# Performance work log

Measured on AMD Instinct MI355X. Metric: run time of the kernel, lower is better.

Reference implementation:

```python
import jax, jax.numpy as jnp
import numpy as np

N_NODES = 50000
N_EDGES = 800000
IN_C, HID_C, OUT_C = 256, 512, 256
DROP_P = 0.5


def _glorot(key, fan_in, fan_out):
    lim = float(np.sqrt(6.0 / (fan_in + fan_out)))
    return jax.random.uniform(key, (fan_in, fan_out), jnp.float32, -lim, lim)


def setup_inputs() -> dict:
    key = jax.random.key(0)
    k_x, k_e, k_w1, k_w2 = jax.random.split(key, 4)
    tensor = jax.random.normal(k_x, (N_NODES, IN_C), dtype=jnp.float32)
    edge_index = jax.random.randint(k_e, (2, N_EDGES), 0, N_NODES, dtype=jnp.int64)
    W1 = _glorot(k_w1, IN_C, HID_C)
    b1 = jnp.zeros((HID_C,), jnp.float32)
    W2 = _glorot(k_w2, HID_C, OUT_C)
    b2 = jnp.zeros((OUT_C,), jnp.float32)
    return {"tensor": tensor, "edge_index": edge_index,
            "W1": W1, "b1": b1, "W2": W2, "b2": b2}


def _gcn_conv(x, W, b, row, col, n_nodes):
    # PyG GCNConv: x' = D^-1/2 (A + I) D^-1/2 (x W) + b
    x = x @ W                                            # [N, F_out]
    # degree over targets including self-loops
    deg = jax.ops.segment_sum(jnp.ones_like(col, dtype=x.dtype), col,
                              num_segments=n_nodes) + 1.0
    dinv = jnp.where(deg > 0, jax.lax.rsqrt(deg), 0.0)   # [N]
    norm = dinv[row] * dinv[col]                         # [E]
    msg = x[row] * norm[:, None]                         # [E, F_out] gather
    out = jax.ops.segment_sum(msg, col, num_segments=n_nodes)  # scatter-add
    out = out + x * (dinv * dinv)[:, None]               # self-loop term
    return out + b


def _dropout(x, key, p=DROP_P):
    keep = jax.random.bernoulli(key, 1.0 - p, x.shape)
    return jnp.where(keep, x / (1.0 - p), 0.0)


def reference(tensor, edge_index, W1, b1, W2, b2):
    row, col = edge_index[0], edge_index[1]
    k1, k2 = jax.random.split(jax.random.key(42))
    x = _gcn_conv(tensor, W1, b1, row, col, N_NODES)
    x = _dropout(jax.nn.relu(x), k1)
    x = _gcn_conv(x, W2, b2, row, col, N_NODES)
    x = _dropout(jax.nn.relu(x), k2)
    return x
```

## Files before the change

kernel.cpp:

```cpp
#include <hip/hip_runtime.h>
#include <stdint.h>


#define N_NODES 50000
#define N_EDGES 800000
#define M_PAD   50048
#define IN_C 256
#define HID_C 512
#define OUT_C 256

typedef __attribute__((ext_vector_type(8))) short bf16x8;
typedef __attribute__((ext_vector_type(4))) float f32x4;

struct U2 { unsigned a, b; };

__host__ __device__ constexpr unsigned rotl32(unsigned x, int d) {
  return (x << d) | (x >> (32 - d));
}

#define TF_ROUND(r) { x0 += x1; x1 = rotl32(x1, (r)); x1 ^= x0; }

__host__ __device__ constexpr U2 threefry2x32(unsigned k0, unsigned k1,
                                              unsigned x0, unsigned x1) {
  unsigned ks2 = k0 ^ k1 ^ 0x1BD11BDAu;
  x0 += k0; x1 += k1;
  TF_ROUND(13) TF_ROUND(15) TF_ROUND(26) TF_ROUND(6)  x0 += k1;  x1 += ks2 + 1u;
  TF_ROUND(17) TF_ROUND(29) TF_ROUND(16) TF_ROUND(24) x0 += ks2; x1 += k0 + 2u;
  TF_ROUND(13) TF_ROUND(15) TF_ROUND(26) TF_ROUND(6)  x0 += k0;  x1 += k1 + 3u;
  TF_ROUND(17) TF_ROUND(29) TF_ROUND(16) TF_ROUND(24) x0 += k1;  x1 += ks2 + 4u;
  TF_ROUND(13) TF_ROUND(15) TF_ROUND(26) TF_ROUND(6)  x0 += ks2; x1 += k0 + 5u;
  return U2{x0, x1};
}

__device__ __forceinline__ float drop_apply(float v, unsigned idx, unsigned k0, unsigned k1) {
  v = fmaxf(v, 0.f);
  U2 r = threefry2x32(k0, k1, 0u, idx);
  unsigned bits = r.a ^ r.b;
  return (bits >> 31) ? 0.f : v * 2.0f;
}

__device__ __forceinline__ ushort f2b(float f) {
  unsigned u = __builtin_bit_cast(unsigned, f);
  unsigned r = (u + 0x7fffu + ((u >> 16) & 1u)) >> 16;
  return (ushort)r;
}
__device__ __forceinline__ float b2f(ushort h) {
  unsigned u = (unsigned)h << 16;
  return __builtin_bit_cast(float, u);
}

__device__ __forceinline__ void gload16(const void* g, void* l) {
  __builtin_amdgcn_global_load_lds(
      (const __attribute__((address_space(1))) void*)g,
      (__attribute__((address_space(3))) void*)l, 16, 0, 0);
}

__global__ void deg_kernel(const int* __restrict__ col, int* __restrict__ cnt, int E) {
  int e = blockIdx.x * 256 + threadIdx.x;
  if (e < E) atomicAdd(&cnt[col[e]], 1);
}

__global__ void dinv_kernel(const int* __restrict__ cnt, float* __restrict__ dinv, int N) {
  int n = blockIdx.x * 256 + threadIdx.x;
  if (n < N) dinv[n] = rsqrtf((float)cnt[n] + 1.0f);
}

__global__ __launch_bounds__(1024) void scan_local(const int* __restrict__ cnt,
                                                   int* __restrict__ indptr,
                                                   int* __restrict__ chunkSums, int n) {
  __shared__ int s[1024];
  int gid = blockIdx.x * 1024 + threadIdx.x;
  int v = (gid < n) ? cnt[gid] : 0;
  s[threadIdx.x] = v;
  __syncthreads();
#pragma unroll
  for (int off = 1; off < 1024; off <<= 1) {
    int t = (threadIdx.x >= off) ? s[threadIdx.x - off] : 0;
    __syncthreads();
    s[threadIdx.x] += t;
    __syncthreads();
  }
  if (gid < n) indptr[gid] = s[threadIdx.x] - v;
  if (threadIdx.x == 1023) chunkSums[blockIdx.x] = s[1023];
}

__global__ void scan_chunks(int* __restrict__ chunkSums, int nChunks) {
  if (threadIdx.x == 0 && blockIdx.x == 0) {
    int acc = 0;
    for (int i = 0; i < nChunks; ++i) { int t = chunkSums[i]; chunkSums[i] = acc; acc += t; }
  }
}

__global__ void add_offsets(int* __restrict__ indptr, const int* __restrict__ chunkSums,
                            int n, int total) {
  int gid = blockIdx.x * 256 + threadIdx.x;
  if (gid < n) indptr[gid] += chunkSums[gid >> 10];
  if (gid == 0) indptr[n] = total;
}

__global__ void build_csr(const int* __restrict__ row, const int* __restrict__ col,
                          const int* __restrict__ indptr, int* __restrict__ cursor,
                          int* __restrict__ srcSorted, int E) {
  int e = blockIdx.x * 256 + threadIdx.x;
  if (e < E) {
    int c = col[e];
    int p = indptr[c] + atomicAdd(&cursor[c], 1);
    srcSorted[p] = row[e];
  }
}

__global__ void cvt_f32_bf16(const float* __restrict__ in, ushort* __restrict__ out, int n4) {
  int i = blockIdx.x * 256 + threadIdx.x;
  if (i < n4) {
    float4 v = *(const float4*)(in + (size_t)i * 4);
    ushort4 o = make_ushort4(f2b(v.x), f2b(v.y), f2b(v.z), f2b(v.w));
    *(ushort4*)(out + (size_t)i * 4) = o;
  }
}

template <int LOGK>
__global__ void wT_kernel(const float* __restrict__ W, ushort* __restrict__ WT, int N, int total) {
  int i = blockIdx.x * 256 + threadIdx.x;
  if (i < total) {
    int k = i & ((1 << LOGK) - 1);
    int n = i >> LOGK;
    WT[i] = f2b(W[(size_t)k * N + n]);
  }
}

template <bool EPI>
__global__ __launch_bounds__(256) void gather_agg16(const ushort* __restrict__ X,
                                                    const int* __restrict__ indptr,
                                                    const int* __restrict__ srcS,
                                                    const float* __restrict__ dinv,
                                                    const float* __restrict__ bias,
                                                    void* __restrict__ outp,
                                                    unsigned char* __restrict__ maskOut,
                                                    unsigned kk0, unsigned kk1, int N) {
  int wid = (blockIdx.x * 256 + threadIdx.x) >> 6;
  int lane = threadIdx.x & 63;
  if (wid >= N) return;
  int beg = __builtin_amdgcn_readfirstlane(indptr[wid]);
  int end = __builtin_amdgcn_readfirstlane(indptr[wid + 1]);
  float dc = dinv[wid];
  const int f0 = lane * 4;
  ushort4 sv = *(const ushort4*)(X + (size_t)wid * 256 + f0);
  float a0 = b2f(sv.x) * dc, a1 = b2f(sv.y) * dc,
        a2 = b2f(sv.z) * dc, a3 = b2f(sv.w) * dc;
  int e = beg;
  for (; e + 2 <= end; e += 2) {
    int r0 = srcS[e], r1 = srcS[e + 1];
    float w0 = dinv[r0], w1 = dinv[r1];
    ushort4 v0 = *(const ushort4*)(X + (size_t)r0 * 256 + f0);
    ushort4 v1 = *(const ushort4*)(X + (size_t)r1 * 256 + f0);
    a0 += b2f(v0.x) * w0; a1 += b2f(v0.y) * w0; a2 += b2f(v0.z) * w0; a3 += b2f(v0.w) * w0;
    a0 += b2f(v1.x) * w1; a1 += b2f(v1.y) * w1; a2 += b2f(v1.z) * w1; a3 += b2f(v1.w) * w1;
  }
  if (e < end) {
    int r0 = srcS[e];
    float w0 = dinv[r0];
    ushort4 v0 = *(const ushort4*)(X + (size_t)r0 * 256 + f0);
    a0 += b2f(v0.x) * w0; a1 += b2f(v0.y) * w0; a2 += b2f(v0.z) * w0; a3 += b2f(v0.w) * w0;
  }
  a0 *= dc; a1 *= dc; a2 *= dc; a3 *= dc;
  if (EPI) {
    unsigned base = (unsigned)wid * 256u + (unsigned)f0;
    a0 = drop_apply(a0 + bias[f0 + 0], base + 0, kk0, kk1);
    a1 = drop_apply(a1 + bias[f0 + 1], base + 1, kk0, kk1);
    a2 = drop_apply(a2 + bias[f0 + 2], base + 2, kk0, kk1);
    a3 = drop_apply(a3 + bias[f0 + 3], base + 3, kk0, kk1);
    *(float4*)((float*)outp + (size_t)wid * 256 + f0) = make_float4(a0, a1, a2, a3);
  } else {
    ushort4 o = make_ushort4(f2b(a0), f2b(a1), f2b(a2), f2b(a3));
    *(ushort4*)((ushort*)outp + (size_t)wid * 256 + f0) = o;
    unsigned gl = (unsigned)wid * 64u + (unsigned)lane;
    unsigned eb = gl * 8u;
    unsigned byte = 0;
#pragma unroll
    for (int j = 0; j < 8; ++j) {
      U2 r = threefry2x32(kk0, kk1, 0u, eb + (unsigned)j);
      byte |= (((r.a ^ r.b) >> 31) & 1u) << j;
    }
    maskOut[gl] = (unsigned char)byte;
  }
}

template <bool EPI>
__global__ __launch_bounds__(256) void gemm_bf16(const ushort* __restrict__ A,
                                                 const ushort* __restrict__ BT,
                                                 ushort* __restrict__ C,
                                                 int M, int K, int N,
                                                 const float* __restrict__ bias,
                                                 const unsigned char* __restrict__ mask) {
  __shared__ __align__(16) ushort lds[4 * 128 * 64];
  const int tid = threadIdx.x;
  const int lane = tid & 63;
  const int wv = tid >> 6;
  const int wr = wv >> 1, wc = wv & 1;
  const int bm = blockIdx.x * 128;
  const int bn = blockIdx.y * 128;

  f32x4 acc[4][4] = {};
  const int xorv = (lane & 7) << 4;

  auto stage = [&](int buf, int k0) {
#pragma unroll
    for (int l = 0; l < 4; ++l) {
      int cid = l * 256 + tid;
      int row = cid >> 3;
      int kcol = ((cid & 7) ^ (row & 7)) * 8;
      gload16(A + (size_t)(bm + row) * K + k0 + kcol, (void*)(lds + buf * 8192 + cid * 8));
      gload16(BT + (size_t)(bn + row) * K + k0 + kcol, (void*)(lds + (2 + buf) * 8192 + cid * 8));
    }
  };

  const int nt = K >> 6;
  stage(0, 0);
  __syncthreads();
  int cur = 0;
  for (int t = 0; t < nt; ++t) {
    if (t + 1 < nt) stage(cur ^ 1, (t + 1) << 6);
    const char* Ab = (const char*)(lds + cur * 8192);
    const char* Bb = (const char*)(lds + (2 + cur) * 8192);
#pragma unroll
    for (int ks = 0; ks < 2; ++ks) {
      bf16x8 af[4], bf[4];
      const int kb = (ks * 64 + (lane >> 4) * 16) ^ xorv;
#pragma unroll
      for (int i = 0; i < 4; ++i) {
        int arow = wr * 64 + i * 16 + (lane & 15);
        af[i] = *(const bf16x8*)(Ab + arow * 128 + kb);
        int brow = wc * 64 + i * 16 + (lane & 15);
        bf[i] = *(const bf16x8*)(Bb + brow * 128 + kb);
      }
#pragma unroll
      for (int m = 0; m < 4; ++m)
#pragma unroll
        for (int n = 0; n < 4; ++n)
          acc[m][n] = __builtin_amdgcn_mfma_f32_16x16x32_bf16(af[m], bf[n], acc[m][n], 0, 0, 0);
    }
    __syncthreads();
    cur ^= 1;
  }

  ushort* Csm = (ushort*)lds;
  const int rowoff = wr * 64 + ((lane >> 4) << 2);
  const int coloff = wc * 64 + (lane & 15);
  float bias_v[4];
  if (EPI) {
#pragma unroll
    for (int n = 0; n < 4; ++n) bias_v[n] = bias[bn + coloff + n * 16];
  }
#pragma unroll
  for (int m = 0; m < 4; ++m) {
#pragma unroll
    for (int r = 0; r < 4; ++r) {
      int lrow = rowoff + m * 16 + r;
      unsigned long long mk = 0;
      if (EPI) {
        unsigned base = (unsigned)(bm + lrow) * (unsigned)N + (unsigned)(bn + wc * 64);
        mk = *(const unsigned long long*)(mask + (base >> 3));
      }
#pragma unroll
      for (int n = 0; n < 4; ++n) {
        float v = acc[m][n][r];
        if (EPI) {
          v = fmaxf(v + bias_v[n], 0.f);
          v = ((mk >> ((lane & 15) + n * 16)) & 1ull) ? 0.f : v * 2.0f;
        }
        Csm[lrow * 132 + coloff + n * 16] = f2b(v);
      }
    }
  }
  __syncthreads();
  {
    int row = tid >> 1, ch = (tid & 1) * 64;
    const ushort* src = Csm + row * 132 + ch;
    ushort* dst = C + (size_t)(bm + row) * N + bn + ch;
#pragma unroll
    for (int j = 0; j < 8; ++j)
      *(bf16x8*)(dst + j * 8) = *(const bf16x8*)(src + j * 8);
  }
}

extern "C" void kernel_launch(void* const* d_in, const int* in_sizes, int n_in,
                              void* d_out, int out_size, void* d_ws, size_t ws_size,
                              hipStream_t stream) {
  const float* x  = (const float*)d_in[0];
  const int*   ei = (const int*)d_in[1];
  const float* W1 = (const float*)d_in[2];
  const float* b1 = (const float*)d_in[3];
  const float* W2 = (const float*)d_in[4];
  const float* b2 = (const float*)d_in[5];
  float* out = (float*)d_out;
  (void)in_sizes; (void)n_in; (void)out_size; (void)ws_size;

  const int* row = ei;
  const int* col = ei + N_EDGES;

  char* ws = (char*)d_ws;
  float*  dinv      = (float*) (ws);
  int*    cnt       = (int*)   (ws + (1u << 18));
  int*    indptr    = (int*)   (ws + (2u << 18));
  int*    cursor    = (int*)   (ws + (3u << 18));
  int*    chunkSums = (int*)   (ws + (1u << 20));
  int*    srcSorted = (int*)   (ws + (1u << 20) + (1u << 16));
  ushort* W1T       = (ushort*)(ws + 5u  * (1u << 20));
  ushort* W2T       = (ushort*)(ws + 5u  * (1u << 20) + (1u << 19));
  unsigned char* mask1 = (unsigned char*)(ws + 6u * (1u << 20));
  ushort* x16       = (ushort*)(ws + 10u * (1u << 20));
  ushort* aggB      = (ushort*)(ws + 36u * (1u << 20));
  ushort* h         = (ushort*)(ws + 64u * (1u << 20));
  ushort* hw2       = (ushort*)(ws + 116u* (1u << 20));

  constexpr U2 K1 = threefry2x32(0u, 42u, 0u, 0u);
  constexpr U2 K2 = threefry2x32(0u, 42u, 0u, 1u);

  hipMemsetAsync(cnt, 0, N_NODES * sizeof(int), stream);
  hipMemsetAsync(cursor, 0, N_NODES * sizeof(int), stream);
  deg_kernel<<<(N_EDGES + 255) / 256, 256, 0, stream>>>(col, cnt, N_EDGES);
  dinv_kernel<<<(N_NODES + 255) / 256, 256, 0, stream>>>(cnt, dinv, N_NODES);
  const int nChunks = (N_NODES + 1023) / 1024;
  scan_local<<<nChunks, 1024, 0, stream>>>(cnt, indptr, chunkSums, N_NODES);
  scan_chunks<<<1, 64, 0, stream>>>(chunkSums, nChunks);
  add_offsets<<<(N_NODES + 255) / 256, 256, 0, stream>>>(indptr, chunkSums, N_NODES, N_EDGES);
  build_csr<<<(N_EDGES + 255) / 256, 256, 0, stream>>>(row, col, indptr, cursor, srcSorted, N_EDGES);

  cvt_f32_bf16<<<(N_NODES * IN_C / 4 + 255) / 256, 256, 0, stream>>>(x, x16, N_NODES * IN_C / 4);
  wT_kernel<8><<<(IN_C * HID_C + 255) / 256, 256, 0, stream>>>(W1, W1T, HID_C, IN_C * HID_C);
  wT_kernel<9><<<(HID_C * OUT_C + 255) / 256, 256, 0, stream>>>(W2, W2T, OUT_C, HID_C * OUT_C);
  hipMemsetAsync(aggB + (size_t)N_NODES * IN_C, 0, (size_t)(M_PAD - N_NODES) * IN_C * 2, stream);

  gather_agg16<false><<<(N_NODES + 3) / 4, 256, 0, stream>>>(
      x16, indptr, srcSorted, dinv, nullptr, aggB, mask1, K1.a, K1.b, N_NODES);
  gemm_bf16<true><<<dim3(M_PAD / 128, HID_C / 128), 256, 0, stream>>>(
      aggB, W1T, h, M_PAD, IN_C, HID_C, b1, mask1);

  gemm_bf16<false><<<dim3(M_PAD / 128, OUT_C / 128), 256, 0, stream>>>(
      h, W2T, hw2, M_PAD, HID_C, OUT_C, nullptr, nullptr);
  gather_agg16<true><<<(N_NODES + 3) / 4, 256, 0, stream>>>(
      hw2, indptr, srcSorted, dinv, b2, out, nullptr, K2.a, K2.b, N_NODES);
}
```

Before: 347.4 us.

## Store gather inputs in 32-feature column chunks for cache-local SpMM

Node features that get gathered (the bf16 input and the second GEMM's output) are stored in eight column-chunked planes of 32 features per node. The gather kernel now assigns each block one chunk, so all blocks working on the same chunk touch a smaller working set that fits in L2. Within a wave, four edge slots run in parallel and are combined with shuffle reductions. The cost is 8x more blocks, each redoing the indptr, srcS and dinv reads. Each block also does narrower 4-byte loads, and the mask generation moves to a subset of blocks.

```diff
diff --git a/kernel.cpp b/kernel.cpp
--- a/kernel.cpp
+++ b/kernel.cpp
@@ -8,6 +8,7 @@
 #define IN_C 256
 #define HID_C 512
 #define OUT_C 256
+#define CH_STRIDE ((size_t)M_PAD * 32)
 
 typedef __attribute__((ext_vector_type(8))) short bf16x8;
 typedef __attribute__((ext_vector_type(4))) float f32x4;
@@ -48,6 +49,12 @@
   unsigned u = (unsigned)h << 16;
   return __builtin_bit_cast(float, u);
 }
+__device__ __forceinline__ float b2f_hi(unsigned u) {
+  return __builtin_bit_cast(float, u & 0xffff0000u);
+}
+__device__ __forceinline__ float b2f_lo(unsigned u) {
+  return __builtin_bit_cast(float, u << 16);
+}
 
 __device__ __forceinline__ void gload16(const void* g, void* l) {
   __builtin_amdgcn_global_load_lds(
@@ -109,12 +116,16 @@
   }
 }
 
-__global__ void cvt_f32_bf16(const float* __restrict__ in, ushort* __restrict__ out, int n4) {
+__global__ void cvt_chunked(const float* __restrict__ in, ushort* __restrict__ Xc, int n4) {
   int i = blockIdx.x * 256 + threadIdx.x;
   if (i < n4) {
+    int n = i >> 6;
+    int fq = (i & 63) * 4;
+    int c = fq >> 5;
+    int fi = fq & 31;
     float4 v = *(const float4*)(in + (size_t)i * 4);
     ushort4 o = make_ushort4(f2b(v.x), f2b(v.y), f2b(v.z), f2b(v.w));
-    *(ushort4*)(out + (size_t)i * 4) = o;
+    *(ushort4*)(Xc + (size_t)c * CH_STRIDE + (size_t)n * 32 + fi) = o;
   }
 }
 
@@ -129,7 +140,7 @@
 }
 
 template <bool EPI>
-__global__ __launch_bounds__(256) void gather_agg16(const ushort* __restrict__ X,
+__global__ __launch_bounds__(256) void gather_chunk(const ushort* __restrict__ Xc,
                                                     const int* __restrict__ indptr,
                                                     const int* __restrict__ srcS,
                                                     const float* __restrict__ dinv,
@@ -137,55 +148,66 @@
                                                     void* __restrict__ outp,
                                                     unsigned char* __restrict__ maskOut,
                                                     unsigned kk0, unsigned kk1, int N) {
-  int wid = (blockIdx.x * 256 + threadIdx.x) >> 6;
-  int lane = threadIdx.x & 63;
-  if (wid >= N) return;
-  int beg = __builtin_amdgcn_readfirstlane(indptr[wid]);
-  int end = __builtin_amdgcn_readfirstlane(indptr[wid + 1]);
-  float dc = dinv[wid];
-  const int f0 = lane * 4;
-  ushort4 sv = *(const ushort4*)(X + (size_t)wid * 256 + f0);
-  float a0 = b2f(sv.x) * dc, a1 = b2f(sv.y) * dc,
-        a2 = b2f(sv.z) * dc, a3 = b2f(sv.w) * dc;
-  int e = beg;
-  for (; e + 2 <= end; e += 2) {
-    int r0 = srcS[e], r1 = srcS[e + 1];
-    float w0 = dinv[r0], w1 = dinv[r1];
-    ushort4 v0 = *(const ushort4*)(X + (size_t)r0 * 256 + f0);
-    ushort4 v1 = *(const ushort4*)(X + (size_t)r1 * 256 + f0);
-    a0 += b2f(v0.x) * w0; a1 += b2f(v0.y) * w0; a2 += b2f(v0.z) * w0; a3 += b2f(v0.w) * w0;
-    a0 += b2f(v1.x) * w1; a1 += b2f(v1.y) * w1; a2 += b2f(v1.z) * w1; a3 += b2f(v1.w) * w1;
-  }
-  if (e < end) {
-    int r0 = srcS[e];
-    float w0 = dinv[r0];
-    ushort4 v0 = *(const ushort4*)(X + (size_t)r0 * 256 + f0);
-    a0 += b2f(v0.x) * w0; a1 += b2f(v0.y) * w0; a2 += b2f(v0.z) * w0; a3 += b2f(v0.w) * w0;
-  }
-  a0 *= dc; a1 *= dc; a2 *= dc; a3 *= dc;
-  if (EPI) {
-    unsigned base = (unsigned)wid * 256u + (unsigned)f0;
-    a0 = drop_apply(a0 + bias[f0 + 0], base + 0, kk0, kk1);
-    a1 = drop_apply(a1 + bias[f0 + 1], base + 1, kk0, kk1);
-    a2 = drop_apply(a2 + bias[f0 + 2], base + 2, kk0, kk1);
-    a3 = drop_apply(a3 + bias[f0 + 3], base + 3, kk0, kk1);
-    *(float4*)((float*)outp + (size_t)wid * 256 + f0) = make_float4(a0, a1, a2, a3);
+  const int bid = blockIdx.x;
+  const int c = bid & 7;
+  const int g = bid >> 3;
+  const int wv = threadIdx.x >> 6;
+  const int lane = threadIdx.x & 63;
+  const int n = g * 4 + wv;
+  if (n >= N) return;
+  const int s = lane >> 4;
+  const int fp = lane & 15;
+  const int beg = __builtin_amdgcn_readfirstlane(indptr[n]);
+  const int end = __builtin_amdgcn_readfirstlane(indptr[n + 1]);
+  const float dc = dinv[n];
+  const ushort* chunk = Xc + (size_t)c * CH_STRIDE;
+
+  float ax = 0.f, ay = 0.f;
+  if (s == 0) {
+    unsigned u = *(const unsigned*)(chunk + (size_t)n * 32 + fp * 2);
+    ax = b2f_lo(u) * dc;
+    ay = b2f_hi(u) * dc;
+  }
+  for (int i = beg + s; i < end; i += 4) {
+    int r = __builtin_nontemporal_load(srcS + i);
+    float w = dinv[r];
+    unsigned u = *(const unsigned*)(chunk + (size_t)r * 32 + fp * 2);
+    ax += b2f_lo(u) * w;
+    ay += b2f_hi(u) * w;
+  }
+  ax += __shfl_xor(ax, 16); ay += __shfl_xor(ay, 16);
+  ax += __shfl_xor(ax, 32); ay += __shfl_xor(ay, 32);
+  ax *= dc; ay *= dc;
+
+  if (!EPI) {
+    if (s == 0) {
+      unsigned o = (unsigned)f2b(ax) | ((unsigned)f2b(ay) << 16);
+      *(unsigned*)((ushort*)outp + (size_t)n * 256 + c * 32 + fp * 2) = o;
+    }
+    if ((g & 7) == c) {
+      unsigned gl = (unsigned)n * 64u + (unsigned)lane;
+      unsigned eb = gl * 8u;
+      unsigned byte = 0;
+#pragma unroll
+      for (int j = 0; j < 8; ++j) {
+        U2 r = threefry2x32(kk0, kk1, 0u, eb + (unsigned)j);
+        byte |= (((r.a ^ r.b) >> 31) & 1u) << j;
+      }
+      maskOut[gl] = (unsigned char)byte;
+    }
   } else {
-    ushort4 o = make_ushort4(f2b(a0), f2b(a1), f2b(a2), f2b(a3));
-    *(ushort4*)((ushort*)outp + (size_t)wid * 256 + f0) = o;
-    unsigned gl = (unsigned)wid * 64u + (unsigned)lane;
-    unsigned eb = gl * 8u;
-    unsigned byte = 0;
-#pragma unroll
-    for (int j = 0; j < 8; ++j) {
-      U2 r = threefry2x32(kk0, kk1, 0u, eb + (unsigned)j);
-      byte |= (((r.a ^ r.b) >> 31) & 1u) << j;
-    }
-    maskOut[gl] = (unsigned char)byte;
-  }
-}
-
-template <bool EPI>
+    float a = __shfl(ax, lane >> 1);
+    float b = __shfl(ay, lane >> 1);
+    float v = (lane & 1) ? b : a;
+    if (lane < 32) {
+      int f = c * 32 + lane;
+      v = drop_apply(v + bias[f], (unsigned)n * 256u + (unsigned)f, kk0, kk1);
+      ((float*)outp)[(size_t)n * 256 + f] = v;
+    }
+  }
+}
+
+template <bool EPI, bool CHUNK_OUT>
 __global__ __launch_bounds__(256) void gemm_bf16(const ushort* __restrict__ A,
                                                  const ushort* __restrict__ BT,
                                                  ushort* __restrict__ C,
@@ -276,10 +298,22 @@
   {
     int row = tid >> 1, ch = (tid & 1) * 64;
     const ushort* src = Csm + row * 132 + ch;
-    ushort* dst = C + (size_t)(bm + row) * N + bn + ch;
-#pragma unroll
-    for (int j = 0; j < 8; ++j)
-      *(bf16x8*)(dst + j * 8) = *(const bf16x8*)(src + j * 8);
+    if (CHUNK_OUT) {
+      int gc = bn + ch;
+#pragma unroll
+      for (int p = 0; p < 2; ++p) {
+        int c = (gc >> 5) + p;
+        ushort* dst = C + (size_t)c * CH_STRIDE + (size_t)(bm + row) * 32;
+#pragma unroll
+        for (int j = 0; j < 4; ++j)
+          *(bf16x8*)(dst + j * 8) = *(const bf16x8*)(src + p * 32 + j * 8);
+      }
+    } else {
+      ushort* dst = C + (size_t)(bm + row) * N + bn + ch;
+#pragma unroll
+      for (int j = 0; j < 8; ++j)
+        *(bf16x8*)(dst + j * 8) = *(const bf16x8*)(src + j * 8);
+    }
   }
 }
 
@@ -308,10 +342,10 @@
   ushort* W1T       = (ushort*)(ws + 5u  * (1u << 20));
   ushort* W2T       = (ushort*)(ws + 5u  * (1u << 20) + (1u << 19));
   unsigned char* mask1 = (unsigned char*)(ws + 6u * (1u << 20));
-  ushort* x16       = (ushort*)(ws + 10u * (1u << 20));
+  ushort* x16c      = (ushort*)(ws + 10u * (1u << 20));
   ushort* aggB      = (ushort*)(ws + 36u * (1u << 20));
   ushort* h         = (ushort*)(ws + 64u * (1u << 20));
-  ushort* hw2       = (ushort*)(ws + 116u* (1u << 20));
+  ushort* hw2c      = (ushort*)(ws + 116u* (1u << 20));
 
   constexpr U2 K1 = threefry2x32(0u, 42u, 0u, 0u);
   constexpr U2 K2 = threefry2x32(0u, 42u, 0u, 1u);
@@ -326,18 +360,20 @@
   add_offsets<<<(N_NODES + 255) / 256, 256, 0, stream>>>(indptr, chunkSums, N_NODES, N_EDGES);
   build_csr<<<(N_EDGES + 255) / 256, 256, 0, stream>>>(row, col, indptr, cursor, srcSorted, N_EDGES);
 
-  cvt_f32_bf16<<<(N_NODES * IN_C / 4 + 255) / 256, 256, 0, stream>>>(x, x16, N_NODES * IN_C / 4);
+  cvt_chunked<<<(N_NODES * IN_C / 4 + 255) / 256, 256, 0, stream>>>(x, x16c, N_NODES * IN_C / 4);
   wT_kernel<8><<<(IN_C * HID_C + 255) / 256, 256, 0, stream>>>(W1, W1T, HID_C, IN_C * HID_C);
   wT_kernel<9><<<(HID_C * OUT_C + 255) / 256, 256, 0, stream>>>(W2, W2T, OUT_C, HID_C * OUT_C);
   hipMemsetAsync(aggB + (size_t)N_NODES * IN_C, 0, (size_t)(M_PAD - N_NODES) * IN_C * 2, stream);
 
-  gather_agg16<false><<<(N_NODES + 3) / 4, 256, 0, stream>>>(
-      x16, indptr, srcSorted, dinv, nullptr, aggB, mask1, K1.a, K1.b, N_NODES);
-  gemm_bf16<true><<<dim3(M_PAD / 128, HID_C / 128), 256, 0, stream>>>(
+  const int gatherGrid = 8 * ((N_NODES + 3) / 4);
+
+  gather_chunk<false><<<gatherGrid, 256, 0, stream>>>(
+      x16c, indptr, srcSorted, dinv, nullptr, aggB, mask1, K1.a, K1.b, N_NODES);
+  gemm_bf16<true, false><<<dim3(M_PAD / 128, HID_C / 128), 256, 0, stream>>>(
       aggB, W1T, h, M_PAD, IN_C, HID_C, b1, mask1);
 
-  gemm_bf16<false><<<dim3(M_PAD / 128, OUT_C / 128), 256, 0, stream>>>(
-      h, W2T, hw2, M_PAD, HID_C, OUT_C, nullptr, nullptr);
-  gather_agg16<true><<<(N_NODES + 3) / 4, 256, 0, stream>>>(
-      hw2, indptr, srcSorted, dinv, b2, out, nullptr, K2.a, K2.b, N_NODES);
-}
+  gemm_bf16<false, true><<<dim3(M_PAD / 128, OUT_C / 128), 256, 0, stream>>>(
+      h, W2T, hw2c, M_PAD, HID_C, OUT_C, nullptr, nullptr);
+  gather_chunk<true><<<gatherGrid, 256, 0, stream>>>(
+      hw2c, indptr, srcSorted, dinv, b2, out, nullptr, K2.a, K2.b, N_NODES);
+}
```

Result: slower. 764.3 us (+120.0%).
